# Optimization experiments

Measured on AMD Instinct MI355X. Metric: run time of the kernel, lower is better.

Reference implementation:

```python
import jax, jax.numpy as jnp
import numpy as np

B, S, HID = 2, 2048, 2048
NH, NKV, HD = 8, 1, 256
G = NH // NKV  # key-value groups
ROPE_BASE = 10000.0


def _rope_tables(seq_len, dim, base=ROPE_BASE):
    inv_freq = 1.0 / (base ** (jnp.arange(0, dim, 2, dtype=jnp.float32) / dim))
    t = jnp.arange(seq_len, dtype=jnp.float32)
    freqs = jnp.outer(t, inv_freq)            # [S, dim/2]
    emb = jnp.concatenate([freqs, freqs], -1)  # [S, dim]
    return jnp.cos(emb), jnp.sin(emb)


def _rotate_half(x):
    x1, x2 = jnp.split(x, 2, axis=-1)
    return jnp.concatenate([-x2, x1], axis=-1)


def setup_inputs() -> dict:
    key = jax.random.key(0)
    ks = jax.random.split(key, 6)
    hidden_states = jax.random.normal(ks[0], (B, S, HID), dtype=jnp.float32)
    # additive causal mask (0 on/below diagonal, -1e9 above)
    causal = jnp.triu(jnp.full((S, S), -1e9, dtype=jnp.float32), k=1)
    attention_mask = jnp.broadcast_to(causal[None, None], (B, 1, S, S))
    sc = 0.02
    Wq = jax.random.normal(ks[1], (HID, NH * HD), dtype=jnp.float32) * sc
    Wk = jax.random.normal(ks[2], (HID, NKV * HD), dtype=jnp.float32) * sc
    Wv = jax.random.normal(ks[3], (HID, NKV * HD), dtype=jnp.float32) * sc
    Wo = jax.random.normal(ks[4], (NH * HD, HID), dtype=jnp.float32) * sc
    return {"hidden_states": hidden_states, "attention_mask": attention_mask,
            "Wq": Wq, "Wk": Wk, "Wv": Wv, "Wo": Wo}


def reference(hidden_states, attention_mask, Wq, Wk, Wv, Wo):
    b, s, _ = hidden_states.shape
    q = (hidden_states @ Wq).reshape(b, s, NH, HD).transpose(0, 2, 1, 3)    # [B,NH,S,D]
    k = (hidden_states @ Wk).reshape(b, s, NKV, HD).transpose(0, 2, 1, 3)   # [B,NKV,S,D]
    v = (hidden_states @ Wv).reshape(b, s, NKV, HD).transpose(0, 2, 1, 3)
    cos, sin = _rope_tables(s, HD)
    cos, sin = cos[None, None], sin[None, None]
    q = q * cos + _rotate_half(q) * sin
    k = k * cos + _rotate_half(k) * sin
    # GQA: broadcast KV over groups instead of repeat_interleave (same math)
    qg = q.reshape(b, NKV, G, s, HD)
    scores = jnp.einsum('bkgqd,bkld->bkgql', qg, k) / np.sqrt(HD)  # [B,NKV,G,S,S]
    scores = scores + attention_mask[:, :, None]                    # mask broadcast over kv/groups
    probs = jax.nn.softmax(scores, axis=-1)
    out = jnp.einsum('bkgql,bkld->bkgqd', probs, v)                 # [B,NKV,G,S,D]
    out = out.reshape(b, NH, s, HD).transpose(0, 2, 1, 3).reshape(b, s, NH * HD)
    return out @ Wo
```

## Files before the change

### kernel.cpp

```cpp
#include <hip/hip_runtime.h>
#include <hip/hip_bf16.h>
#include <cstdint>
#include <cstddef>

#define DEVI __device__ __forceinline__

typedef __attribute__((ext_vector_type(8))) short short8;
typedef __attribute__((ext_vector_type(4))) float f32x4;

constexpr int BB = 2, SS = 2048, HID = 2048, NH = 8, HD = 256;
constexpr int M_TOT = BB * SS;
constexpr int RTOT = BB * NH * SS;
constexpr float SM_SCALE_LOG2 = 0.09016844005556021f;

DEVI unsigned short f2bf(float f) {
  union { float f; unsigned int u; } v; v.f = f;
  unsigned int u = v.u;
  unsigned int r = (u + 0x7FFFu + ((u >> 16) & 1u)) >> 16;
  return (unsigned short)r;
}

DEVI float bf2f(unsigned short u) {
  union { unsigned int i; float f; } v; v.i = ((unsigned int)u) << 16;
  return v.f;
}

DEVI void gload_lds16(const void* g, void* l) {
  __builtin_amdgcn_global_load_lds(
      (const __attribute__((address_space(1))) unsigned int*)g,
      (__attribute__((address_space(3))) unsigned int*)l, 16, 0, 0);
}

__global__ void convert_f32_bf16(const float* __restrict__ in,
                                 unsigned short* __restrict__ out, int n8) {
  const int i = blockIdx.x * blockDim.x + threadIdx.x;
  if (i >= n8) return;
  const f32x4* p = (const f32x4*)in;
  f32x4 a = p[i * 2], b = p[i * 2 + 1];
  short8 o;
#pragma unroll
  for (int j = 0; j < 4; ++j) {
    o[j] = (short)f2bf(a[j]);
    o[j + 4] = (short)f2bf(b[j]);
  }
  ((short8*)out)[i] = o;
}

__global__ void transpose_w(const float* __restrict__ W,
                            unsigned short* __restrict__ Wt, int K, int N) {
  __shared__ float t[32][33];
  const int n0 = blockIdx.x * 32, k0 = blockIdx.y * 32;
  const int c = threadIdx.x & 31, r8 = threadIdx.x >> 5;
#pragma unroll
  for (int i = 0; i < 4; ++i) {
    const int r = r8 + i * 8;
    t[r][c] = W[(size_t)(k0 + r) * N + n0 + c];
  }
  __syncthreads();
#pragma unroll
  for (int i = 0; i < 4; ++i) {
    const int r = r8 + i * 8;
    Wt[(size_t)(n0 + r) * K + k0 + c] = f2bf(t[c][r]);
  }
}

__global__ void rope_table(float* __restrict__ ct, float* __restrict__ st) {
  const int i = blockIdx.x * blockDim.x + threadIdx.x;
  const int s = i >> 7, d = i & 127;
  const float inv = __expf(-(float)d * (9.210340371976184f / 128.0f));
  const float ang = (float)s * inv;
  float sn, cs;
  sincosf(ang, &sn, &cs);
  ct[i] = cs;
  st[i] = sn;
}

__global__ void rope_apply8(unsigned short* __restrict__ X, const float* __restrict__ ct,
                            const float* __restrict__ st, int heads, int stride, int total16) {
  const int i = blockIdx.x * blockDim.x + threadIdx.x;
  if (i >= total16) return;
  const int d0 = (i & 15) * 8;
  const int t = i >> 4;
  const int hh = t % heads;
  const int row = t / heads;
  const int s = row & (SS - 1);
  const size_t base = (size_t)row * stride + (size_t)hh * HD + d0;
  short8 q1 = *(const short8*)&X[base];
  short8 q2 = *(const short8*)&X[base + 128];
  const float* ctr = ct + s * 128 + d0;
  const float* str = st + s * 128 + d0;
  f32x4 c0 = *(const f32x4*)ctr, c1 = *(const f32x4*)(ctr + 4);
  f32x4 s0 = *(const f32x4*)str, s1 = *(const f32x4*)(str + 4);
  short8 o1, o2;
#pragma unroll
  for (int j = 0; j < 8; ++j) {
    const float a = bf2f((unsigned short)q1[j]);
    const float b = bf2f((unsigned short)q2[j]);
    const float cs = (j < 4) ? c0[j] : c1[j - 4];
    const float sn = (j < 4) ? s0[j] : s1[j - 4];
    o1[j] = (short)f2bf(a * cs - b * sn);
    o2[j] = (short)f2bf(b * cs + a * sn);
  }
  *(short8*)&X[base] = o1;
  *(short8*)&X[base + 128] = o2;
}

template <int WMODE>
__global__ __launch_bounds__(256)
void gemm_bt(const unsigned short* __restrict__ A,
             const unsigned short* __restrict__ Bt,
             void* __restrict__ Cp, void* __restrict__ Cp2, void* __restrict__ Cp3,
             int N, int K) {
  __shared__ unsigned short As[128 * 64];
  __shared__ unsigned short Bs[128 * 64];
  const int tid = threadIdx.x;
  const int wid = tid >> 6, lane = tid & 63;
  const int wr = wid >> 1, wc = wid & 1;
  const int l15 = lane & 15, lg = lane >> 4;
  const unsigned lid = blockIdx.y * gridDim.x + blockIdx.x;
  const unsigned cpx = (gridDim.x * gridDim.y) >> 3;
  const unsigned swz = (lid & 7) * cpx + (lid >> 3);
  const int m0 = (int)(swz / gridDim.x) * 128, n0 = (int)(swz % gridDim.x) * 128;
  const int lrow = lane >> 3, lch = lane & 7;
  f32x4 acc[4][4];
#pragma unroll
  for (int i = 0; i < 4; ++i)
#pragma unroll
    for (int j = 0; j < 4; ++j) acc[i][j] = f32x4{0.f, 0.f, 0.f, 0.f};
  const unsigned short* Ab = A + (size_t)m0 * K;
  const unsigned short* Bb = Bt + (size_t)n0 * K;
  for (int k0 = 0; k0 < K; k0 += 64) {
    __syncthreads();
#pragma unroll
    for (int i = 0; i < 4; ++i) {
      const int r0 = wid * 32 + i * 8;
      const int r = r0 + lrow;
      gload_lds16(Ab + (size_t)r * K + k0 + ((lch ^ (r & 7)) * 8), &As[r0 * 64]);
      gload_lds16(Bb + (size_t)r * K + k0 + ((lch ^ (r & 7)) * 8), &Bs[r0 * 64]);
    }
    asm volatile("s_waitcnt vmcnt(0)" ::: "memory");
    __syncthreads();
#pragma unroll
    for (int kk = 0; kk < 2; ++kk) {
      short8 a[4], b[4];
#pragma unroll
      for (int m = 0; m < 4; ++m) {
        const int row = wr * 64 + m * 16 + l15;
        a[m] = *(const short8*)&As[row * 64 + (((kk * 4 + lg) ^ (row & 7)) * 8)];
      }
#pragma unroll
      for (int n = 0; n < 4; ++n) {
        const int row = wc * 64 + n * 16 + l15;
        b[n] = *(const short8*)&Bs[row * 64 + (((kk * 4 + lg) ^ (row & 7)) * 8)];
      }
#pragma unroll
      for (int m = 0; m < 4; ++m)
#pragma unroll
        for (int n = 0; n < 4; ++n)
          acc[m][n] = __builtin_amdgcn_mfma_f32_16x16x32_bf16(a[m], b[n], acc[m][n], 0, 0, 0);
    }
  }
  const int row0 = m0 + wr * 64 + lg * 4;
  const int col0 = n0 + wc * 64 + l15;
#pragma unroll
  for (int m = 0; m < 4; ++m)
#pragma unroll
    for (int n = 0; n < 4; ++n)
#pragma unroll
      for (int r = 0; r < 4; ++r) {
        const int row = row0 + m * 16 + r;
        const int col = col0 + n * 16;
        const float v = acc[m][n][r];
        if (WMODE == 1) {
          ((float*)Cp)[(size_t)row * N + col] = v;
        } else {
          if (col < 2048)
            ((unsigned short*)Cp)[(size_t)row * 2048 + col] = f2bf(v);
          else if (col < 2304)
            ((unsigned short*)Cp2)[(size_t)row * 256 + (col - 2048)] = f2bf(v);
          else
            ((unsigned short*)Cp3)[((size_t)((row >> 11) * HD + (col - 2304))) * SS + (row & (SS - 1))] = f2bf(v);
        }
      }
}

__global__ __launch_bounds__(512)
void attn_split(const unsigned short* __restrict__ Q,
                const unsigned short* __restrict__ Kc,
                const unsigned short* __restrict__ Vt,
                unsigned short* __restrict__ Opart, float* __restrict__ Ml) {
  __shared__ unsigned short Ks[64 * 256];
  __shared__ unsigned short Vs[256 * 64];
  const int tid = threadIdx.x;
  const int wid = tid >> 6, lane = tid & 63;
  const int l15 = lane & 15, lg = lane >> 4;
  const int pi = (int)blockIdx.x >> 1, s = (int)blockIdx.x & 1;
  const int h = blockIdx.y, b = blockIdx.z;
  const int qtA = pi, qtB = 15 - pi;

  short8 qf[8];
  f32x4 acc[16];
  float mrow[4], lrow[4];

  auto load_q = [&](int qt) {
    const int qrow = qt * 128 + wid * 16 + l15;
    const size_t qbase = ((size_t)(b * SS + qrow)) * (NH * HD) + (size_t)h * HD;
#pragma unroll
    for (int c = 0; c < 8; ++c)
      qf[c] = *(const short8*)&Q[qbase + c * 32 + lg * 8];
#pragma unroll
    for (int n = 0; n < 16; ++n) acc[n] = f32x4{0.f, 0.f, 0.f, 0.f};
#pragma unroll
    for (int r = 0; r < 4; ++r) { mrow[r] = -3e38f; lrow[r] = 0.f; }
  };

  auto write_part = [&](int qt) {
    const size_t rbase = ((size_t)(b * NH + h)) * SS + qt * 128 + wid * 16 + lg * 4;
#pragma unroll
    for (int n = 0; n < 16; ++n)
#pragma unroll
      for (int r = 0; r < 4; ++r)
        Opart[((size_t)s * RTOT + rbase + r) * 256 + n * 16 + l15] = f2bf(acc[n][r]);
    if (l15 == 0) {
#pragma unroll
      for (int r = 0; r < 4; ++r)
        ((float2*)Ml)[(size_t)s * RTOT + rbase + r] = float2{mrow[r], lrow[r]};
    }
  };

  auto stage = [&](int kv0) {
#pragma unroll
    for (int j = 0; j < 4; ++j) {
      {
        const int r0 = wid * 8 + j * 2;
        const int r = r0 + (lane >> 5), c = lane & 31;
        gload_lds16(Kc + ((size_t)(b * SS + kv0 + r)) * HD + ((c ^ (r & 7)) * 8),
                    &Ks[r0 * 256]);
      }
      {
        const int r0 = (wid * 4 + j) * 8;
        const int r = r0 + (lane >> 3), c = lane & 7;
        gload_lds16(Vt + ((size_t)(b * HD + r)) * SS + kv0 + ((c ^ (r & 7)) * 8),
                    &Vs[r0 * 64]);
      }
    }
  };

  auto kv_of = [&](int i) {
    const int j = (i <= qtA) ? i : (i - qtA - 1);
    return (s + 2 * j) * 64;
  };

  load_q(qtA);
  for (int i = 0; i < 17; ++i) {
    const int kv0 = kv_of(i);
    __syncthreads();
    stage(kv0);
    asm volatile("s_waitcnt vmcnt(0)" ::: "memory");
    __syncthreads();
    if (i == qtA + 1) {
      write_part(qtA);
      load_q(qtB);
    }
    const int qt = (i <= qtA) ? qtA : qtB;
    const bool active = kv0 <= qt * 128 + wid * 16 + 15;

    f32x4 sf[4];
    if (active) {
      __builtin_amdgcn_s_setprio(1);
#pragma unroll
      for (int t = 0; t < 4; ++t) {
        f32x4 sv = {0.f, 0.f, 0.f, 0.f};
        const int kvr = t * 16 + l15;
        const char* krow = (const char*)Ks + kvr * 512;
        const int sw = (kvr & 7) << 4;
#pragma unroll
        for (int c = 0; c < 8; ++c) {
          short8 bf = *(const short8*)(krow + ((c * 64 + lg * 16) ^ sw));
          sv = __builtin_amdgcn_mfma_f32_16x16x32_bf16(qf[c], bf, sv, 0, 0, 0);
        }
        sf[t] = sv;
      }
      __builtin_amdgcn_s_setprio(0);
    }
    __syncthreads();

    if (active) {
      float pm[4] = {-3e38f, -3e38f, -3e38f, -3e38f};
      const int qr0 = qt * 128 + wid * 16 + lg * 4;
#pragma unroll
      for (int t = 0; t < 4; ++t) {
        const int kvc = kv0 + t * 16 + l15;
#pragma unroll
        for (int r = 0; r < 4; ++r) {
          float v = sf[t][r] * SM_SCALE_LOG2;
          v = (kvc > qr0 + r) ? -3e38f : v;
          sf[t][r] = v;
          pm[r] = fmaxf(pm[r], v);
        }
      }
      float scale[4];
      float growth = -3e38f;
#pragma unroll
      for (int r = 0; r < 4; ++r) {
        float v = pm[r];
        v = fmaxf(v, __shfl_xor(v, 1));
        v = fmaxf(v, __shfl_xor(v, 2));
        v = fmaxf(v, __shfl_xor(v, 4));
        v = fmaxf(v, __shfl_xor(v, 8));
        pm[r] = v;
        growth = fmaxf(growth, v - mrow[r]);
      }
      const bool norescale = __all(growth <= 0.f);
#pragma unroll
      for (int r = 0; r < 4; ++r) {
        const float mn = norescale ? mrow[r] : fmaxf(mrow[r], pm[r]);
        scale[r] = norescale ? 1.f : exp2f(mrow[r] - mn);
        mrow[r] = mn;
        float sum = 0.f;
#pragma unroll
        for (int t = 0; t < 4; ++t) {
          const float p = exp2f(sf[t][r] - mn);
          sf[t][r] = p;
          sum += p;
        }
        sum += __shfl_xor(sum, 1);
        sum += __shfl_xor(sum, 2);
        sum += __shfl_xor(sum, 4);
        sum += __shfl_xor(sum, 8);
        lrow[r] = lrow[r] * scale[r] + sum;
      }
      if (!norescale) {
#pragma unroll
        for (int n = 0; n < 16; ++n)
#pragma unroll
          for (int r = 0; r < 4; ++r) acc[n][r] *= scale[r];
      }

      char* pw = (char*)&Ks[wid * 1024];
#pragma unroll
      for (int t = 0; t < 4; ++t)
#pragma unroll
        for (int r = 0; r < 4; ++r) {
          const int q = lg * 4 + r;
          *(unsigned short*)(pw + q * 128 + (((t * 16 + l15) * 2) ^ ((q & 7) << 4))) =
              f2bf(sf[t][r]);
        }
      asm volatile("s_waitcnt lgkmcnt(0)" ::: "memory");
      short8 pf[2];
      {
        const char* pr = pw + l15 * 128;
        const int sw = (l15 & 7) << 4;
        pf[0] = *(const short8*)(pr + ((lg * 16) ^ sw));
        pf[1] = *(const short8*)(pr + ((64 + lg * 16) ^ sw));
      }
      __builtin_amdgcn_s_setprio(1);
#pragma unroll
      for (int n = 0; n < 16; ++n) {
        const int dr = n * 16 + l15;
        const char* vrow = (const char*)Vs + dr * 128;
        const int sw = (dr & 7) << 4;
        short8 v0 = *(const short8*)(vrow + ((lg * 16) ^ sw));
        short8 v1 = *(const short8*)(vrow + ((64 + lg * 16) ^ sw));
        acc[n] = __builtin_amdgcn_mfma_f32_16x16x32_bf16(pf[0], v0, acc[n], 0, 0, 0);
        acc[n] = __builtin_amdgcn_mfma_f32_16x16x32_bf16(pf[1], v1, acc[n], 0, 0, 0);
      }
      __builtin_amdgcn_s_setprio(0);
    }
  }
  write_part(qtB);
}

__global__ void merge_splits(const unsigned short* __restrict__ Opart,
                             const float* __restrict__ Ml,
                             unsigned short* __restrict__ AO) {
  const int gid = blockIdx.x * 256 + threadIdx.x;
  const int ridx = gid >> 5;
  const int d0 = (gid & 31) * 8;
  const float2 ab0 = ((const float2*)Ml)[ridx];
  const float2 ab1 = ((const float2*)Ml)[RTOT + ridx];
  const float M = fmaxf(ab0.x, ab1.x);
  const float w0 = exp2f(ab0.x - M), w1 = exp2f(ab1.x - M);
  const float inv = 1.f / (w0 * ab0.y + w1 * ab1.y);
  const short8 p0 = *(const short8*)&Opart[(size_t)ridx * 256 + d0];
  const short8 p1 = *(const short8*)&Opart[((size_t)RTOT + ridx) * 256 + d0];
  const int b = ridx >> 14, rem = ridx & 16383;
  const int h = rem >> 11, srow = rem & 2047;
  short8 o;
#pragma unroll
  for (int j = 0; j < 8; ++j)
    o[j] = (short)f2bf((w0 * bf2f((unsigned short)p0[j]) +
                        w1 * bf2f((unsigned short)p1[j])) * inv);
  *(short8*)(AO + ((size_t)(b * SS + srow)) * (NH * HD) + (size_t)h * HD + d0) = o;
}

__global__ __launch_bounds__(256)
void attn_fb(const unsigned short* __restrict__ Q,
             const unsigned short* __restrict__ Kc,
             const unsigned short* __restrict__ Vt,
             unsigned short* __restrict__ AO) {
  __shared__ unsigned short Ks[2][64 * 256];
  __shared__ unsigned short Vs[2][256 * 64];
  __shared__ unsigned short Ps[4][1024];
  const int tid = threadIdx.x;
  const int wid = tid >> 6, lane = tid & 63;
  const int l15 = lane & 15, lg = lane >> 4;
  const int qtA = (int)blockIdx.x;
  const int qtB = 31 - qtA;
  const int h = blockIdx.y, b = blockIdx.z;

  short8 qf[8];
  f32x4 acc[16];
  float mrow[4], lrow[4];

  auto load_q = [&](int qt) {
    const int qrow = qt * 64 + wid * 16 + l15;
    const size_t qbase = ((size_t)(b * SS + qrow)) * (NH * HD) + (size_t)h * HD;
#pragma unroll
    for (int c = 0; c < 8; ++c)
      qf[c] = *(const short8*)&Q[qbase + c * 32 + lg * 8];
#pragma unroll
    for (int n = 0; n < 16; ++n) acc[n] = f32x4{0.f, 0.f, 0.f, 0.f};
#pragma unroll
    for (int r = 0; r < 4; ++r) { mrow[r] = -3e38f; lrow[r] = 0.f; }
  };

  auto write_o = [&](int qt) {
    float invl[4];
#pragma unroll
    for (int r = 0; r < 4; ++r) invl[r] = 1.f / lrow[r];
    const int orow0 = b * SS + qt * 64 + wid * 16 + lg * 4;
#pragma unroll
    for (int n = 0; n < 16; ++n)
#pragma unroll
      for (int r = 0; r < 4; ++r)
        AO[(size_t)(orow0 + r) * (NH * HD) + (size_t)h * HD + n * 16 + l15] =
            f2bf(acc[n][r] * invl[r]);
  };

  auto stage = [&](int buf, int kv0) {
    unsigned short* KsB = &Ks[buf][0];
    unsigned short* VsB = &Vs[buf][0];
#pragma unroll
    for (int j = 0; j < 8; ++j) {
      {
        const int r0 = wid * 16 + j * 2;
        const int r = r0 + (lane >> 5), c = lane & 31;
        gload_lds16(Kc + ((size_t)(b * SS + kv0 + r)) * HD + ((c ^ (r & 7)) * 8),
                    &KsB[r0 * 256]);
      }
      {
        const int r0 = (wid * 8 + j) * 8;
        const int r = r0 + (lane >> 3), c = lane & 7;
        gload_lds16(Vt + ((size_t)(b * HD + r)) * SS + kv0 + ((c ^ (r & 7)) * 8),
                    &VsB[r0 * 64]);
      }
    }
  };

  auto compute = [&](int buf, int qt, int kv0) {
    const int wmax = qt * 64 + wid * 16 + 15;
    if (kv0 > wmax) return;
    const unsigned short* KsB = &Ks[buf][0];
    const unsigned short* VsB = &Vs[buf][0];
    f32x4 sf[4];
#pragma unroll
    for (int t = 0; t < 4; ++t) {
      f32x4 sv = {0.f, 0.f, 0.f, 0.f};
      const int kvr = t * 16 + l15;
      const char* krow = (const char*)KsB + kvr * 512;
      const int sw = (kvr & 7) << 4;
#pragma unroll
      for (int c = 0; c < 8; ++c) {
        short8 bf = *(const short8*)(krow + ((c * 64 + lg * 16) ^ sw));
        sv = __builtin_amdgcn_mfma_f32_16x16x32_bf16(qf[c], bf, sv, 0, 0, 0);
      }
      sf[t] = sv;
    }
    float pm[4] = {-3e38f, -3e38f, -3e38f, -3e38f};
    const int qr0 = qt * 64 + wid * 16 + lg * 4;
#pragma unroll
    for (int t = 0; t < 4; ++t) {
      const int kvc = kv0 + t * 16 + l15;
#pragma unroll
      for (int r = 0; r < 4; ++r) {
        float v = sf[t][r] * 0.0625f;
        v = (kvc > qr0 + r) ? -3e38f : v;
        sf[t][r] = v;
        pm[r] = fmaxf(pm[r], v);
      }
    }
    float scale[4];
    float growth = -3e38f;
#pragma unroll
    for (int r = 0; r < 4; ++r) {
      float v = pm[r];
      v = fmaxf(v, __shfl_xor(v, 1));
      v = fmaxf(v, __shfl_xor(v, 2));
      v = fmaxf(v, __shfl_xor(v, 4));
      v = fmaxf(v, __shfl_xor(v, 8));
      pm[r] = v;
      growth = fmaxf(growth, v - mrow[r]);
    }
    const bool norescale = __all(growth <= 0.f);
#pragma unroll
    for (int r = 0; r < 4; ++r) {
      const float mn = norescale ? mrow[r] : fmaxf(mrow[r], pm[r]);
      scale[r] = norescale ? 1.f : __expf(mrow[r] - mn);
      mrow[r] = mn;
      float sum = 0.f;
#pragma unroll
      for (int t = 0; t < 4; ++t) {
        const float p = __expf(sf[t][r] - mn);
        sf[t][r] = p;
        sum += p;
      }
      sum += __shfl_xor(sum, 1);
      sum += __shfl_xor(sum, 2);
      sum += __shfl_xor(sum, 4);
      sum += __shfl_xor(sum, 8);
      lrow[r] = lrow[r] * scale[r] + sum;
    }
    if (!norescale) {
#pragma unroll
      for (int n = 0; n < 16; ++n)
#pragma unroll
        for (int r = 0; r < 4; ++r) acc[n][r] *= scale[r];
    }
    char* pw = (char*)&Ps[wid][0];
#pragma unroll
    for (int t = 0; t < 4; ++t)
#pragma unroll
      for (int r = 0; r < 4; ++r) {
        const int q = lg * 4 + r;
        *(unsigned short*)(pw + q * 128 + (((t * 16 + l15) * 2) ^ ((q & 7) << 4))) =
            f2bf(sf[t][r]);
      }
    asm volatile("s_waitcnt lgkmcnt(0)" ::: "memory");
    short8 pf[2];
    {
      const char* pr = pw + l15 * 128;
      const int sw = (l15 & 7) << 4;
      pf[0] = *(const short8*)(pr + ((lg * 16) ^ sw));
      pf[1] = *(const short8*)(pr + ((64 + lg * 16) ^ sw));
    }
#pragma unroll
    for (int n = 0; n < 16; ++n) {
      const int dr = n * 16 + l15;
      const char* vrow = (const char*)VsB + dr * 128;
      const int sw = (dr & 7) << 4;
      short8 v0 = *(const short8*)(vrow + ((lg * 16) ^ sw));
      short8 v1 = *(const short8*)(vrow + ((64 + lg * 16) ^ sw));
      acc[n] = __builtin_amdgcn_mfma_f32_16x16x32_bf16(pf[0], v0, acc[n], 0, 0, 0);
      acc[n] = __builtin_amdgcn_mfma_f32_16x16x32_bf16(pf[1], v1, acc[n], 0, 0, 0);
    }
  };

  const int nA = qtA + 1;
  load_q(qtA);
  int curq = qtA;
  stage(0, 0);
  asm volatile("s_waitcnt vmcnt(0)" ::: "memory");
  __syncthreads();
  int buf = 0;
  for (int i = 0; i < 33; ++i) {
    const int t0 = (i >= nA) ? (i - nA) : i;
    if (i + 1 < 33) {
      const int t0n = (i + 1 >= nA) ? (i + 1 - nA) : (i + 1);
      stage(buf ^ 1, t0n * 64);
    }
    if (i >= nA && curq == qtA) {
      write_o(qtA);
      load_q(qtB);
      curq = qtB;
    }
    compute(buf, curq, t0 * 64);
    asm volatile("s_waitcnt vmcnt(0)" ::: "memory");
    __syncthreads();
    buf ^= 1;
  }
  write_o(qtB);
}

extern "C" void kernel_launch(void* const* d_in, const int* in_sizes, int n_in,
                              void* d_out, int out_size, void* d_ws, size_t ws_size,
                              hipStream_t stream) {
  (void)in_sizes; (void)n_in; (void)out_size;
  const float* hs = (const float*)d_in[0];
  const float* Wq = (const float*)d_in[2];
  const float* Wk = (const float*)d_in[3];
  const float* Wv = (const float*)d_in[4];
  const float* Wo = (const float*)d_in[5];

  char* ws = (char*)d_ws;
  size_t off = 0;
  auto alloc = [&](size_t bytes) -> void* {
    void* p = ws + off;
    off += (bytes + 255) & ~(size_t)255;
    return p;
  };
  unsigned short* Xb  = (unsigned short*)alloc((size_t)M_TOT * HID * 2);
  unsigned short* WqT = (unsigned short*)alloc((size_t)2048 * 2048 * 2);
  unsigned short* WkT = (unsigned short*)alloc((size_t)256 * 2048 * 2);
  unsigned short* WvT = (unsigned short*)alloc((size_t)256 * 2048 * 2);
  unsigned short* WoT = (unsigned short*)alloc((size_t)2048 * 2048 * 2);
  unsigned short* Qb  = (unsigned short*)alloc((size_t)M_TOT * 2048 * 2);
  unsigned short* Kb  = (unsigned short*)alloc((size_t)M_TOT * 256 * 2);
  unsigned short* Vtw = (unsigned short*)alloc((size_t)M_TOT * 256 * 2);
  float* ct = (float*)alloc((size_t)SS * 128 * 4);
  float* st = (float*)alloc((size_t)SS * 128 * 4);
  unsigned short* Opart = (unsigned short*)alloc((size_t)2 * RTOT * 256 * 2);
  float* Mlb = (float*)alloc((size_t)2 * RTOT * 2 * 4);
  const bool use_split = ws_size >= off;
  unsigned short* AO = Xb;

  convert_f32_bf16<<<M_TOT * HID / 8 / 256, 256, 0, stream>>>(hs, Xb, M_TOT * HID / 8);
  transpose_w<<<dim3(2048 / 32, 2048 / 32), 256, 0, stream>>>(Wq, WqT, 2048, 2048);
  transpose_w<<<dim3(256 / 32, 2048 / 32), 256, 0, stream>>>(Wk, WkT, 2048, 256);
  transpose_w<<<dim3(256 / 32, 2048 / 32), 256, 0, stream>>>(Wv, WvT, 2048, 256);
  transpose_w<<<dim3(2048 / 32, 2048 / 32), 256, 0, stream>>>(Wo, WoT, 2048, 2048);
  rope_table<<<SS * 128 / 256, 256, 0, stream>>>(ct, st);

  gemm_bt<4><<<dim3(2560 / 128, M_TOT / 128), 256, 0, stream>>>(Xb, WqT, Qb, Kb, Vtw, 2560, 2048);

  rope_apply8<<<(M_TOT * NH * 16) / 256, 256, 0, stream>>>(Qb, ct, st, NH, 2048, M_TOT * NH * 16);
  rope_apply8<<<(M_TOT * 16) / 256, 256, 0, stream>>>(Kb, ct, st, 1, 256, M_TOT * 16);

  if (use_split) {
    attn_split<<<dim3(16, NH, BB), 512, 0, stream>>>(Qb, Kb, Vtw, Opart, Mlb);
    merge_splits<<<RTOT * 32 / 256, 256, 0, stream>>>(Opart, Mlb, AO);
  } else {
    attn_fb<<<dim3(16, NH, BB), 256, 0, stream>>>(Qb, Kb, Vtw, AO);
  }

  gemm_bt<1><<<dim3(2048 / 128, M_TOT / 128), 256, 0, stream>>>(AO, WoT, d_out, nullptr, nullptr, 2048, 2048);
}
```

Measured before the change: 235.6 us.

## Split attention KV range four ways instead of two and merge four partials

The split-KV attention kernel now divides each query-tile pair's key/value blocks across four blocks (interleaved stride 4) instead of two, doubling the grid to 512 blocks. Per-block step counts are computed from the causal extent, and the merge kernel combines four partial outputs with log-sum-exp weights. The goal is more parallelism and better CU occupancy on a 256-CU device, at the cost of twice the partial-output workspace and more merge traffic. If the workspace is too small, execution falls back to the non-split kernel.

```diff
diff --git a/kernel.cpp b/kernel.cpp
--- a/kernel.cpp
+++ b/kernel.cpp
@@ -194,9 +194,12 @@
   const int tid = threadIdx.x;
   const int wid = tid >> 6, lane = tid & 63;
   const int l15 = lane & 15, lg = lane >> 4;
-  const int pi = (int)blockIdx.x >> 1, s = (int)blockIdx.x & 1;
+  const int pi = (int)blockIdx.x >> 2, s = (int)blockIdx.x & 3;
   const int h = blockIdx.y, b = blockIdx.z;
   const int qtA = pi, qtB = 15 - pi;
+  const int jA = (2 * qtA + 1 - s >= 0) ? (((2 * qtA + 1 - s) >> 2) + 1) : 0;
+  const int jB = ((31 - 2 * qtA - s) >> 2) + 1;
+  const int nsteps = jA + jB;
 
   short8 qf[8];
   f32x4 acc[16];
@@ -246,23 +249,23 @@
     }
   };
 
-  auto kv_of = [&](int i) {
-    const int j = (i <= qtA) ? i : (i - qtA - 1);
-    return (s + 2 * j) * 64;
-  };
-
   load_q(qtA);
-  for (int i = 0; i < 17; ++i) {
-    const int kv0 = kv_of(i);
+  if (jA == 0) {
+    write_part(qtA);
+    load_q(qtB);
+  }
+  for (int i = 0; i < nsteps; ++i) {
+    const int j = (i < jA) ? i : (i - jA);
+    const int kv0 = (s + 4 * j) * 64;
     __syncthreads();
     stage(kv0);
     asm volatile("s_waitcnt vmcnt(0)" ::: "memory");
     __syncthreads();
-    if (i == qtA + 1) {
+    if (i == jA && jA > 0) {
       write_part(qtA);
       load_q(qtB);
     }
-    const int qt = (i <= qtA) ? qtA : qtB;
+    const int qt = (i < jA) ? qtA : qtB;
     const bool active = kv0 <= qt * 128 + wid * 16 + 15;
 
     f32x4 sf[4];
@@ -377,20 +380,31 @@
   const int gid = blockIdx.x * 256 + threadIdx.x;
   const int ridx = gid >> 5;
   const int d0 = (gid & 31) * 8;
-  const float2 ab0 = ((const float2*)Ml)[ridx];
-  const float2 ab1 = ((const float2*)Ml)[RTOT + ridx];
-  const float M = fmaxf(ab0.x, ab1.x);
-  const float w0 = exp2f(ab0.x - M), w1 = exp2f(ab1.x - M);
-  const float inv = 1.f / (w0 * ab0.y + w1 * ab1.y);
-  const short8 p0 = *(const short8*)&Opart[(size_t)ridx * 256 + d0];
-  const short8 p1 = *(const short8*)&Opart[((size_t)RTOT + ridx) * 256 + d0];
+  float2 ab[4];
+#pragma unroll
+  for (int s = 0; s < 4; ++s) ab[s] = ((const float2*)Ml)[(size_t)s * RTOT + ridx];
+  float M = fmaxf(fmaxf(ab[0].x, ab[1].x), fmaxf(ab[2].x, ab[3].x));
+  float w[4], denom = 0.f;
+#pragma unroll
+  for (int s = 0; s < 4; ++s) {
+    w[s] = exp2f(ab[s].x - M);
+    denom += w[s] * ab[s].y;
+  }
+  const float inv = 1.f / denom;
+  short8 p[4];
+#pragma unroll
+  for (int s = 0; s < 4; ++s)
+    p[s] = *(const short8*)&Opart[((size_t)s * RTOT + ridx) * 256 + d0];
   const int b = ridx >> 14, rem = ridx & 16383;
   const int h = rem >> 11, srow = rem & 2047;
   short8 o;
 #pragma unroll
-  for (int j = 0; j < 8; ++j)
-    o[j] = (short)f2bf((w0 * bf2f((unsigned short)p0[j]) +
-                        w1 * bf2f((unsigned short)p1[j])) * inv);
+  for (int j = 0; j < 8; ++j) {
+    float v = 0.f;
+#pragma unroll
+    for (int s = 0; s < 4; ++s) v += w[s] * bf2f((unsigned short)p[s][j]);
+    o[j] = (short)f2bf(v * inv);
+  }
   *(short8*)(AO + ((size_t)(b * SS + srow)) * (NH * HD) + (size_t)h * HD + d0) = o;
 }
 
@@ -609,8 +623,8 @@
   unsigned short* Vtw = (unsigned short*)alloc((size_t)M_TOT * 256 * 2);
   float* ct = (float*)alloc((size_t)SS * 128 * 4);
   float* st = (float*)alloc((size_t)SS * 128 * 4);
-  unsigned short* Opart = (unsigned short*)alloc((size_t)2 * RTOT * 256 * 2);
-  float* Mlb = (float*)alloc((size_t)2 * RTOT * 2 * 4);
+  unsigned short* Opart = (unsigned short*)alloc((size_t)4 * RTOT * 256 * 2);
+  float* Mlb = (float*)alloc((size_t)4 * RTOT * 2 * 4);
   const bool use_split = ws_size >= off;
   unsigned short* AO = Xb;
 
@@ -627,7 +641,7 @@
   rope_apply8<<<(M_TOT * 16) / 256, 256, 0, stream>>>(Kb, ct, st, 1, 256, M_TOT * 16);
 
   if (use_split) {
-    attn_split<<<dim3(16, NH, BB), 512, 0, stream>>>(Qb, Kb, Vtw, Opart, Mlb);
+    attn_split<<<dim3(32, NH, BB), 512, 0, stream>>>(Qb, Kb, Vtw, Opart, Mlb);
     merge_splits<<<RTOT * 32 / 256, 256, 0, stream>>>(Opart, Mlb, AO);
   } else {
     attn_fb<<<dim3(16, NH, BB), 256, 0, stream>>>(Qb, Kb, Vtw, AO);
```

After: 251.7 us. 1.07x slower.
